# Optimization experiments

Hardware: AMD Instinct MI355X
Metric: run time of the kernel (lower is better)

Reference implementation:

```python
import jax, jax.numpy as jnp
import numpy as np

B, S, H = 8, 2048, 2048

def setup_inputs() -> dict:
    key = jax.random.key(0)
    ks = jax.random.split(key, 7)
    return {
        "time_decay": jax.random.normal(ks[0], (H,), dtype=jnp.float32),
        "key": jax.random.normal(ks[1], (B, S, H), dtype=jnp.float32),
        "time_first": jax.random.normal(ks[2], (H,), dtype=jnp.float32),
        "value": jax.random.normal(ks[3], (B, S, H), dtype=jnp.float32),
        "max_state": jax.random.normal(ks[4], (B, H), dtype=jnp.float32),
        "num_state": jax.random.normal(ks[5], (B, H), dtype=jnp.float32),
        "den_state": jax.random.uniform(ks[6], (B, H), dtype=jnp.float32),
    }

def _wkv(time_decay, k, time_first, v, max_state, num_state, den_state):
    f32 = jnp.float32
    td = -jnp.exp(time_decay.astype(f32))          # [H]
    tf = time_first.astype(f32)                    # [H]
    k = k.astype(f32)
    v = v.astype(f32)

    def step(carry, kv_t):
        m, num, den = carry                        # each [B,H]
        kt, vt = kv_t                              # each [B,H]
        # output branch: include time_first bonus
        mo = jnp.maximum(m, kt + tf)
        e1o = jnp.exp(m - mo)
        e2o = jnp.exp(kt + tf - mo)
        out = (e1o * num + e2o * vt) / (e1o * den + e2o)
        # state branch: apply decay
        ms = jnp.maximum(m + td, kt)
        e1s = jnp.exp(m + td - ms)
        e2s = jnp.exp(kt - ms)
        return (ms, e1s * num + e2s * vt, e1s * den + e2s), out

    carry0 = (max_state.astype(f32), num_state.astype(f32), den_state.astype(f32))
    # scan over time: move seq axis to front -> [S,B,H]
    (m, num, den), outs = jax.lax.scan(
        step, carry0, (jnp.swapaxes(k, 0, 1), jnp.swapaxes(v, 0, 1)))
    output = jnp.swapaxes(outs, 0, 1)              # [B,S,H]
    return output, m, num, den

def reference(time_decay, key, time_first, value, max_state, num_state, den_state):
    return _wkv(time_decay, key, time_first, value, max_state, num_state, den_state)
```

## Files before the change

### kernel.cpp

```cpp
#include <hip/hip_runtime.h>


#define TILE 128
#define NW   16
#define SUB  (TILE / NW)

#define VMW0  asm volatile("s_waitcnt vmcnt(0)" ::: "memory")
#define VMW8  asm volatile("s_waitcnt vmcnt(8)" ::: "memory")
#define BARR  asm volatile("s_waitcnt lgkmcnt(0)\n\ts_barrier" ::: "memory")

__device__ __forceinline__ float ex2(float x)  { return __builtin_amdgcn_exp2f(x); }
__device__ __forceinline__ float rcpf(float x) { return __builtin_amdgcn_rcpf(x); }

__device__ __forceinline__ void dma16(const float* g, float* l) {
    __builtin_amdgcn_global_load_lds(
        (const __attribute__((address_space(1))) unsigned int*)g,
        (__attribute__((address_space(3))) unsigned int*)l, 16, 0, 0);
}

__global__ __launch_bounds__(1024)
void wkv_fwd(const float* __restrict__ td_in, const float* __restrict__ kin,
             const float* __restrict__ tf_in, const float* __restrict__ vin,
             const float* __restrict__ m0, const float* __restrict__ n0,
             const float* __restrict__ d0,
             float* __restrict__ out, float* __restrict__ m_out,
             float* __restrict__ n_out, float* __restrict__ dn_out,
             int B, int S, int H)
{
    __shared__ float kbuf[2][TILE][64];
    __shared__ float vbuf[2][TILE][64];
    __shared__ float smry[NW][3][64];
    __shared__ float cry[2][3][64];

    const int tid  = threadIdx.x;
    const int lane = tid & 63;
    const int w    = tid >> 6;

    const int bpb = H >> 6;
    const int b   = blockIdx.x / bpb;
    const int hb  = (blockIdx.x - b * bpb) << 6;
    const int h   = hb + lane;
    const int g   = b * H + h;

    constexpr float Cc = 1.4426950408889634f;
    constexpr float IC = 0.6931471805599453f;

    const float tds  = -ex2(td_in[h] * Cc) * Cc;
    const float tfs  = tf_in[h] * Cc;
    const float dseg = tds * (float)SUB;

    if (w == 0) {
        cry[0][0][lane] = m0[g] * Cc;
        cry[0][1][lane] = n0[g];
        cry[0][2][lane] = d0[g];
    }

    const size_t base = (size_t)b * (size_t)S * (size_t)H + (size_t)hb;
    const float* gk = kin + base;
    const float* gv = vin + base;
    float*       go = out + base;

    const int sub = lane >> 4;
    const int c4  = (lane & 15) << 2;

    const int ntiles = S / TILE;

    #pragma unroll
    for (int i = 0; i < SUB / 4; ++i) {
        const int r = w * SUB + i * 4;
        dma16(gk + (size_t)(r + sub) * H + c4, &kbuf[0][r][0]);
        dma16(gv + (size_t)(r + sub) * H + c4, &vbuf[0][r][0]);
    }

    float M = 0.f, N = 0.f, D = 0.f;

    for (int it = 0; it < ntiles; ++it) {
        const int p = it & 1;
        if (it == 0) { VMW0; } else { VMW8; }
        BARR;

        if (it + 1 < ntiles) {
            const int np = p ^ 1;
            const size_t t1 = (size_t)(it + 1) * TILE;
            #pragma unroll
            for (int i = 0; i < SUB / 4; ++i) {
                const int r = w * SUB + i * 4;
                dma16(gk + (t1 + r + sub) * (size_t)H + c4, &kbuf[np][r][0]);
                dma16(gv + (t1 + r + sub) * (size_t)H + c4, &vbuf[np][r][0]);
            }
        }

        float lm = -1e30f, ln = 0.f, ldn = 0.f;
        #pragma unroll
        for (int j = 0; j < SUB; ++j) {
            const float kt  = kbuf[p][w * SUB + j][lane] * Cc;
            const float vt  = vbuf[p][w * SUB + j][lane];
            const float mpd = lm + tds;
            const float d   = mpd - kt;
            const float e   = ex2(0.f - fabsf(d));
            const bool  c   = d >= 0.f;
            const float e1  = c ? 1.f : e;
            const float e2  = c ? e : 1.f;
            ln  = e1 * ln  + e2 * vt;
            ldn = e1 * ldn + e2;
            lm  = fmaxf(mpd, kt);
        }
        smry[w][0][lane] = lm;
        smry[w][1][lane] = ln;
        smry[w][2][lane] = ldn;
        BARR;

        M = cry[p][0][lane];
        N = cry[p][1][lane];
        D = cry[p][2][lane];
        for (int j = 0; j < w; ++j) {
            const float Md = M + dseg;
            const float sm = smry[j][0][lane];
            const float d  = Md - sm;
            const float e  = ex2(0.f - fabsf(d));
            const bool  c  = d >= 0.f;
            const float a  = c ? 1.f : e;
            const float bb = c ? e : 1.f;
            N = a * N + bb * smry[j][1][lane];
            D = a * D + bb * smry[j][2][lane];
            M = fmaxf(Md, sm);
        }

        float* po = go + ((size_t)it * TILE + (size_t)w * SUB) * (size_t)H;
        #pragma unroll
        for (int j = 0; j < SUB; ++j) {
            const float kt  = kbuf[p][w * SUB + j][lane] * Cc;
            const float vt  = vbuf[p][w * SUB + j][lane];
            const float ktf = kt + tfs;
            const float dd  = M - ktf;
            const float eo  = ex2(0.f - fabsf(dd));
            const bool  co  = dd >= 0.f;
            const float e1o = co ? 1.f : eo;
            const float e2o = co ? eo : 1.f;
            po[(size_t)j * H + lane] =
                (e1o * N + e2o * vt) * rcpf(e1o * D + e2o);
            const float mpd = M + tds;
            const float ds_ = mpd - kt;
            const float es  = ex2(0.f - fabsf(ds_));
            const bool  cs  = ds_ >= 0.f;
            const float e1s = cs ? 1.f : es;
            const float e2s = cs ? es : 1.f;
            N = e1s * N + e2s * vt;
            D = e1s * D + e2s;
            M = fmaxf(mpd, kt);
        }

        if (w == NW - 1) {
            cry[p ^ 1][0][lane] = M;
            cry[p ^ 1][1][lane] = N;
            cry[p ^ 1][2][lane] = D;
        }
    }

    if (w == NW - 1) {
        m_out[g]  = M * IC;
        n_out[g]  = N;
        dn_out[g] = D;
    }
}

__global__ __launch_bounds__(64)
void wkv_fwd_serial(const float* __restrict__ td_in, const float* __restrict__ kin,
                    const float* __restrict__ tf_in, const float* __restrict__ vin,
                    const float* __restrict__ m0, const float* __restrict__ n0,
                    const float* __restrict__ d0,
                    float* __restrict__ out, float* __restrict__ m_out,
                    float* __restrict__ n_out, float* __restrict__ dn_out,
                    int B, int S, int H)
{
    const int g = blockIdx.x * 64 + threadIdx.x;
    if (g >= B * H) return;
    const int b = g / H;
    const int h = g - b * H;
    constexpr float Cc = 1.4426950408889634f, IC = 0.6931471805599453f;
    const float tds = -ex2(td_in[h] * Cc) * Cc;
    const float tfs = tf_in[h] * Cc;
    float M = m0[g] * Cc, N = n0[g], D = d0[g];
    const size_t base = (size_t)b * S * H + h;
    for (int t = 0; t < S; ++t) {
        const float kt  = kin[base + (size_t)t * H] * Cc;
        const float vt  = vin[base + (size_t)t * H];
        const float ktf = kt + tfs;
        const float mo  = fmaxf(M, ktf);
        const float e1o = ex2(M - mo), e2o = ex2(ktf - mo);
        out[base + (size_t)t * H] = (e1o * N + e2o * vt) * rcpf(e1o * D + e2o);
        const float mpd = M + tds;
        const float ms  = fmaxf(mpd, kt);
        const float e1s = ex2(mpd - ms), e2s = ex2(kt - ms);
        N = e1s * N + e2s * vt;
        D = e1s * D + e2s;
        M = ms;
    }
    m_out[g] = M * IC; n_out[g] = N; dn_out[g] = D;
}

extern "C" void kernel_launch(void* const* d_in, const int* in_sizes, int n_in,
                              void* d_out, int out_size, void* d_ws, size_t ws_size,
                              hipStream_t stream)
{
    const float* time_decay = (const float*)d_in[0];
    const float* key        = (const float*)d_in[1];
    const float* time_first = (const float*)d_in[2];
    const float* value      = (const float*)d_in[3];
    const float* max_state  = (const float*)d_in[4];
    const float* num_state  = (const float*)d_in[5];
    const float* den_state  = (const float*)d_in[6];

    const int H  = in_sizes[0];
    const int BH = in_sizes[4];
    const int B  = BH / H;
    const int S  = in_sizes[1] / BH;

    float* out    = (float*)d_out;
    float* m_out  = out + (size_t)B * (size_t)S * (size_t)H;
    float* n_out  = m_out + BH;
    float* dn_out = n_out + BH;

    if ((H % 64 == 0) && (S % TILE == 0)) {
        const int grid = BH / 64;
        wkv_fwd<<<grid, 1024, 0, stream>>>(time_decay, key, time_first, value,
                                           max_state, num_state, den_state,
                                           out, m_out, n_out, dn_out, B, S, H);
    } else {
        const int grid = (BH + 63) / 64;
        wkv_fwd_serial<<<grid, 64, 0, stream>>>(time_decay, key, time_first, value,
                                                max_state, num_state, den_state,
                                                out, m_out, n_out, dn_out, B, S, H);
    }
}
```

Before: 345.6 us.

## Drop per-tile barrier and parallelize output pass using register-held local prefixes

Each warp now keeps its k/v values and per-step local scan prefixes in registers. Outputs are computed by combining the warp's incoming carry with each stored prefix, so the output loop no longer carries a serial dependency. The summary buffer is double-buffered and the last warp computes the next tile's carry right after the inter-warp combine, which removes the leading barrier in each tile iteration. This trades extra registers for a shorter critical path and one fewer barrier per tile.

```diff
diff --git a/kernel.cpp b/kernel.cpp
--- a/kernel.cpp
+++ b/kernel.cpp
@@ -29,7 +29,7 @@
 {
     __shared__ float kbuf[2][TILE][64];
     __shared__ float vbuf[2][TILE][64];
-    __shared__ float smry[NW][3][64];
+    __shared__ float smry[2][NW][3][64];
     __shared__ float cry[2][3][64];
 
     const int tid  = threadIdx.x;
@@ -72,12 +72,11 @@
         dma16(gv + (size_t)(r + sub) * H + c4, &vbuf[0][r][0]);
     }
 
-    float M = 0.f, N = 0.f, D = 0.f;
+    float fM = 0.f, fN = 0.f, fD = 0.f;
 
     for (int it = 0; it < ntiles; ++it) {
         const int p = it & 1;
         if (it == 0) { VMW0; } else { VMW8; }
-        BARR;
 
         if (it + 1 < ntiles) {
             const int np = p ^ 1;
@@ -90,77 +89,98 @@
             }
         }
 
-        float lm = -1e30f, ln = 0.f, ldn = 0.f;
+        float kt[SUB], vt[SUB];
+        float plm[SUB - 1], pln[SUB - 1], pld[SUB - 1];
+        float lm = -1e30f, ln = 0.f, ld = 0.f;
         #pragma unroll
         for (int j = 0; j < SUB; ++j) {
-            const float kt  = kbuf[p][w * SUB + j][lane] * Cc;
-            const float vt  = vbuf[p][w * SUB + j][lane];
+            kt[j] = kbuf[p][w * SUB + j][lane] * Cc;
+            vt[j] = vbuf[p][w * SUB + j][lane];
             const float mpd = lm + tds;
-            const float d   = mpd - kt;
-            const float e   = ex2(0.f - fabsf(d));
+            const float d   = mpd - kt[j];
+            const float e   = ex2(-fabsf(d));
             const bool  c   = d >= 0.f;
             const float e1  = c ? 1.f : e;
             const float e2  = c ? e : 1.f;
-            ln  = e1 * ln  + e2 * vt;
-            ldn = e1 * ldn + e2;
-            lm  = fmaxf(mpd, kt);
-        }
-        smry[w][0][lane] = lm;
-        smry[w][1][lane] = ln;
-        smry[w][2][lane] = ldn;
+            ln  = e1 * ln  + e2 * vt[j];
+            ld  = e1 * ld  + e2;
+            lm  = fmaxf(mpd, kt[j]);
+            if (j < SUB - 1) { plm[j] = lm; pln[j] = ln; pld[j] = ld; }
+        }
+        smry[p][w][0][lane] = lm;
+        smry[p][w][1][lane] = ln;
+        smry[p][w][2][lane] = ld;
         BARR;
 
-        M = cry[p][0][lane];
-        N = cry[p][1][lane];
-        D = cry[p][2][lane];
+        float M = cry[p][0][lane];
+        float N = cry[p][1][lane];
+        float D = cry[p][2][lane];
         for (int j = 0; j < w; ++j) {
             const float Md = M + dseg;
-            const float sm = smry[j][0][lane];
+            const float sm = smry[p][j][0][lane];
             const float d  = Md - sm;
-            const float e  = ex2(0.f - fabsf(d));
+            const float e  = ex2(-fabsf(d));
             const bool  c  = d >= 0.f;
             const float a  = c ? 1.f : e;
             const float bb = c ? e : 1.f;
-            N = a * N + bb * smry[j][1][lane];
-            D = a * D + bb * smry[j][2][lane];
+            N = a * N + bb * smry[p][j][1][lane];
+            D = a * D + bb * smry[p][j][2][lane];
             M = fmaxf(Md, sm);
         }
 
+        if (w == NW - 1) {
+            const float Md = M + dseg;
+            const float d  = Md - lm;
+            const float e  = ex2(-fabsf(d));
+            const bool  c  = d >= 0.f;
+            const float a  = c ? 1.f : e;
+            const float bb = c ? e : 1.f;
+            fN = a * N + bb * ln;
+            fD = a * D + bb * ld;
+            fM = fmaxf(Md, lm);
+            cry[p ^ 1][0][lane] = fM;
+            cry[p ^ 1][1][lane] = fN;
+            cry[p ^ 1][2][lane] = fD;
+        }
+
         float* po = go + ((size_t)it * TILE + (size_t)w * SUB) * (size_t)H;
+        {
+            const float ktf = kt[0] + tfs;
+            const float dd  = M - ktf;
+            const float eo  = ex2(-fabsf(dd));
+            const bool  co  = dd >= 0.f;
+            const float e1o = co ? 1.f : eo;
+            const float e2o = co ? eo : 1.f;
+            po[lane] = (e1o * N + e2o * vt[0]) * rcpf(fmaf(e1o, D, e2o));
+        }
+        float Md = M;
         #pragma unroll
-        for (int j = 0; j < SUB; ++j) {
-            const float kt  = kbuf[p][w * SUB + j][lane] * Cc;
-            const float vt  = vbuf[p][w * SUB + j][lane];
-            const float ktf = kt + tfs;
-            const float dd  = M - ktf;
-            const float eo  = ex2(0.f - fabsf(dd));
+        for (int j = 1; j < SUB; ++j) {
+            Md += tds;
+            const float sm = plm[j - 1];
+            const float dl = Md - sm;
+            const float e  = ex2(-fabsf(dl));
+            const bool  c  = dl >= 0.f;
+            const float a  = c ? 1.f : e;
+            const float bb = c ? e : 1.f;
+            const float Nc = a * N + bb * pln[j - 1];
+            const float Dc = a * D + bb * pld[j - 1];
+            const float Mc = fmaxf(Md, sm);
+            const float ktf = kt[j] + tfs;
+            const float dd  = Mc - ktf;
+            const float eo  = ex2(-fabsf(dd));
             const bool  co  = dd >= 0.f;
             const float e1o = co ? 1.f : eo;
             const float e2o = co ? eo : 1.f;
             po[(size_t)j * H + lane] =
-                (e1o * N + e2o * vt) * rcpf(e1o * D + e2o);
-            const float mpd = M + tds;
-            const float ds_ = mpd - kt;
-            const float es  = ex2(0.f - fabsf(ds_));
-            const bool  cs  = ds_ >= 0.f;
-            const float e1s = cs ? 1.f : es;
-            const float e2s = cs ? es : 1.f;
-            N = e1s * N + e2s * vt;
-            D = e1s * D + e2s;
-            M = fmaxf(mpd, kt);
-        }
-
-        if (w == NW - 1) {
-            cry[p ^ 1][0][lane] = M;
-            cry[p ^ 1][1][lane] = N;
-            cry[p ^ 1][2][lane] = D;
+                (e1o * Nc + e2o * vt[j]) * rcpf(fmaf(e1o, Dc, e2o));
         }
     }
 
     if (w == NW - 1) {
-        m_out[g]  = M * IC;
-        n_out[g]  = N;
-        dn_out[g] = D;
+        m_out[g]  = fM * IC;
+        n_out[g]  = fN;
+        dn_out[g] = fD;
     }
 }
 
```

New measurement: 338.8 us. No clear change (-2.0%).
